# Kernel optimization log

Measured on AMD Instinct MI355X. Metric: run time of the kernel, lower is better.

The kernel has to match this reference:

```python
import jax, jax.numpy as jnp
import numpy as np

NEG_SLOPE = 0.2
EPS = 1e-10

B, N, F_IN = 2, 20000, 128
H, D = 4, 32
E = 640000


def setup_inputs() -> dict:
    key = jax.random.key(0)
    k1, k2, k3, k4, k5 = jax.random.split(key, 5)
    x = jax.random.normal(k1, (B, N, F_IN), dtype=jnp.float32)
    edge_index = jax.random.randint(k2, (2, E), 0, N, dtype=jnp.int64)
    W = jax.random.normal(k3, (H * D, F_IN), dtype=jnp.float32) * (1.0 / np.sqrt(F_IN))
    a_src = jax.random.normal(k4, (H, D), dtype=jnp.float32) * (1.0 / np.sqrt(D))
    a_dst = jax.random.normal(k5, (H, D), dtype=jnp.float32) * (1.0 / np.sqrt(D))
    return {"x": x, "edge_index": edge_index, "W": W, "a_src": a_src, "a_dst": a_dst}


def reference(x, edge_index, W, a_src, a_dst):
    # x: (B, N, F_IN); edge_index: (2, E); W: (H*D, F_IN)
    Bs, Ns, _ = x.shape
    h = (x @ W.T).reshape(Bs, Ns, H, D)          # (B, N, H, D)
    src = edge_index[0]
    dst = edge_index[1]

    h_src = h[:, src]                            # (B, E, H, D) gather
    e_src = jnp.einsum('behd,hd->beh', h_src, a_src)
    e_dst = jnp.einsum('behd,hd->beh', h[:, dst], a_dst)
    e = jax.nn.leaky_relu(e_src + e_dst, NEG_SLOPE)  # (B, E, H)

    # segment softmax over destination nodes (segments on leading axis)
    e_t = jnp.moveaxis(e, 1, 0)                  # (E, B, H)
    max_n = jax.ops.segment_max(e_t, dst, num_segments=Ns)   # (N, B, H)
    exp_e = jnp.exp(e_t - max_n[dst])            # (E, B, H)
    sum_n = jax.ops.segment_sum(exp_e, dst, num_segments=Ns)  # (N, B, H)
    alpha = exp_e / (sum_n[dst] + EPS)           # (E, B, H)

    messages = alpha[..., None] * jnp.moveaxis(h_src, 1, 0)  # (E, B, H, D)
    out = jax.ops.segment_sum(messages, dst, num_segments=Ns)  # (N, B, H, D)
    out = jnp.moveaxis(out, 0, 1).reshape(Bs, Ns, H * D)       # concat heads
    return out
```

## Files before the change

### kernel.cpp

```cpp
#include <hip/hip_runtime.h>
#include <math.h>

#define N_NODES 20000
#define N_B 2
#define N_H 4
#define N_D 32
#define N_F 128
#define N_E 640000
#define BNH (N_B * N_NODES * N_H)

#define GEMM_BLOCKS 625
#define P1_BLOCKS 250
#define EPB 2560
#define NBINS 157
#define NODE_CAP 96
#define TRS 136
#define LOG2E 1.44269504088896f

typedef __attribute__((ext_vector_type(8))) short short8v;
typedef __attribute__((ext_vector_type(4))) float floatx4;

__device__ __forceinline__ unsigned short f2bf(float f) {
  unsigned u = __float_as_uint(f);
  return (unsigned short)((u + 0x7FFFu + ((u >> 16) & 1u)) >> 16);
}

__global__ __launch_bounds__(256) void fused_gemm_p1(
    const float* __restrict__ X, const float* __restrict__ W,
    const int* __restrict__ EI, const float* __restrict__ a_src,
    const float* __restrict__ a_dst, unsigned short* __restrict__ HbI,
    float* __restrict__ sI, float* __restrict__ sdI,
    int* __restrict__ cntB, int* __restrict__ prefB,
    unsigned* __restrict__ blockEdges) {
  __shared__ union {
    struct {
      unsigned short WbS[128 * 128];
      unsigned short Tr[4][16 * TRS];
    } g;
    struct {
      int hist[NBINS];
      int pref[NBINS];
      int wsum[4];
      unsigned buf[EPB];
    } p;
  } sm;
  const int tid = threadIdx.x;

  if (blockIdx.x >= GEMM_BLOCKS) {
    const int pb = blockIdx.x - GEMM_BLOCKS;
    const int e0 = pb * EPB;
    for (int t = tid; t < NBINS; t += 256) sm.p.hist[t] = 0;
    __syncthreads();
    for (int k = 0; k < EPB; k += 256) {
      const int d = EI[N_E + e0 + k + tid];
      atomicAdd(&sm.p.hist[d >> 7], 1);
    }
    __syncthreads();
    {
      const int w = tid >> 6, lane = tid & 63;
      int v = 0, incl = 0;
      if (tid < NBINS) v = sm.p.hist[tid];
      if (w < 3) {
        incl = v;
#pragma unroll
        for (int off = 1; off < 64; off <<= 1) {
          int t2 = __shfl_up(incl, off);
          if (lane >= off) incl += t2;
        }
        if (lane == 63) sm.p.wsum[w] = incl;
      }
      __syncthreads();
      if (tid < NBINS) {
        int add = 0;
        if (w >= 1) add += sm.p.wsum[0];
        if (w >= 2) add += sm.p.wsum[1];
        sm.p.pref[tid] = incl - v + add;
      }
      __syncthreads();
    }
    for (int t = tid; t < NBINS; t += 256) {
      cntB[pb * NBINS + t] = sm.p.hist[t];
      prefB[pb * NBINS + t] = sm.p.pref[t];
      sm.p.hist[t] = sm.p.pref[t];
    }
    __syncthreads();
    for (int k = 0; k < EPB; k += 256) {
      const int i = e0 + k + tid;
      const int d = EI[N_E + i];
      const int s = EI[i];
      const int pos = atomicAdd(&sm.p.hist[d >> 7], 1);
      sm.p.buf[pos] = (unsigned)(((d & 127) << 16) | s);
    }
    __syncthreads();
    for (int k = tid; k < EPB; k += 256)
      blockEdges[(size_t)pb * EPB + k] = sm.p.buf[k];
    return;
  }

  {
    const int o = tid >> 1;
    const int khalf = (tid & 1) * 64;
#pragma unroll
    for (int c = 0; c < 8; ++c) {
      const int k0 = khalf + c * 8;
      const float4 w0 = *(const float4*)&W[(size_t)o * 128 + k0];
      const float4 w1 = *(const float4*)&W[(size_t)o * 128 + k0 + 4];
      union { unsigned short us[8]; uint4 v; } pk;
      pk.us[0] = f2bf(w0.x); pk.us[1] = f2bf(w0.y);
      pk.us[2] = f2bf(w0.z); pk.us[3] = f2bf(w0.w);
      pk.us[4] = f2bf(w1.x); pk.us[5] = f2bf(w1.y);
      pk.us[6] = f2bf(w1.z); pk.us[7] = f2bf(w1.w);
      const int chunk = (k0 >> 3) ^ (o & 15);
      *(uint4*)&sm.g.WbS[o * 128 + chunk * 8] = pk.v;
    }
  }
  __syncthreads();

  const int wv = tid >> 6, lane = tid & 63;
  const int l15 = lane & 15;
  const int row0 = blockIdx.x * 64 + wv * 16;
  const int arow = row0 + l15;
  const int kg = lane >> 4;

  float as[8], ad[8];
#pragma unroll
  for (int cf = 0; cf < 8; ++cf) {
    as[cf] = a_src[cf * 16 + l15];
    ad[cf] = a_dst[cf * 16 + l15];
  }

  short8v afr[4];
#pragma unroll
  for (int kc = 0; kc < 4; ++kc) {
    const size_t xb = (size_t)arow * 128 + kc * 32 + kg * 8;
    const float4 x0 = *(const float4*)&X[xb];
    const float4 x1 = *(const float4*)&X[xb + 4];
    afr[kc][0] = (short)f2bf(x0.x); afr[kc][1] = (short)f2bf(x0.y);
    afr[kc][2] = (short)f2bf(x0.z); afr[kc][3] = (short)f2bf(x0.w);
    afr[kc][4] = (short)f2bf(x1.x); afr[kc][5] = (short)f2bf(x1.y);
    afr[kc][6] = (short)f2bf(x1.z); afr[kc][7] = (short)f2bf(x1.w);
  }

  floatx4 acc[8];
#pragma unroll
  for (int cf = 0; cf < 8; ++cf) acc[cf] = (floatx4){0.f, 0.f, 0.f, 0.f};

#pragma unroll
  for (int kc = 0; kc < 4; ++kc) {
#pragma unroll
    for (int cf = 0; cf < 8; ++cf) {
      const int o = cf * 16 + l15;
      const int chunk = (kc * 4 + kg) ^ l15;
      const short8v bfr = *(const short8v*)&sm.g.WbS[o * 128 + chunk * 8];
      acc[cf] = __builtin_amdgcn_mfma_f32_16x16x32_bf16(afr[kc], bfr, acc[cf], 0, 0, 0);
    }
  }

  {
    float ps[4][4], pd[4][4];
#pragma unroll
    for (int j = 0; j < 4; ++j)
#pragma unroll
      for (int h = 0; h < 4; ++h) {
        float vs = acc[2 * h][j] * as[2 * h] + acc[2 * h + 1][j] * as[2 * h + 1];
        float vd = acc[2 * h][j] * ad[2 * h] + acc[2 * h + 1][j] * ad[2 * h + 1];
#pragma unroll
        for (int m = 1; m <= 8; m <<= 1) {
          vs += __shfl_xor(vs, m);
          vd += __shfl_xor(vd, m);
        }
        ps[j][h] = vs * LOG2E; pd[j][h] = vd * LOG2E;
      }
    if (l15 == 0) {
#pragma unroll
      for (int j = 0; j < 4; ++j) {
        const int m = row0 + kg * 4 + j;
        const int node = (m < N_NODES) ? m : m - N_NODES;
        const int boff = (m < N_NODES) ? 0 : 4;
#pragma unroll
        for (int h = 0; h < 4; ++h) {
          sI[node * 8 + boff + h] = ps[j][h];
          sdI[node * 8 + boff + h] = pd[j][h];
        }
      }
    }
  }

#pragma unroll
  for (int cf = 0; cf < 8; ++cf)
#pragma unroll
    for (int j = 0; j < 4; ++j)
      sm.g.Tr[wv][((kg << 2) + j) * TRS + cf * 16 + l15] = f2bf(acc[cf][j]);
#pragma unroll
  for (int it = 0; it < 4; ++it) {
    const int r = it * 4 + kg;
    const int m = row0 + r;
    const size_t base2 =
        (m < N_NODES) ? (size_t)m * 256 : (size_t)(m - N_NODES) * 256 + 128;
    const uint4 v = *(const uint4*)&sm.g.Tr[wv][r * TRS + l15 * 8];
    *(uint4*)&HbI[base2 + l15 * 8] = v;
  }
}

__global__ __launch_bounds__(256) void bin_kernel(
    const unsigned* __restrict__ blockEdges, const int* __restrict__ cntB,
    const int* __restrict__ prefB, unsigned short* __restrict__ bucket,
    int* __restrict__ count) {
  __shared__ unsigned short list[128][NODE_CAP];
  __shared__ int cnt[128];
  const int bin = blockIdx.x;
  const int tid = threadIdx.x;
  if (tid < 128) cnt[tid] = 0;
  __syncthreads();
  for (int b = tid; b < P1_BLOCKS; b += 256) {
    const int c = cntB[b * NBINS + bin];
    const int p0 = prefB[b * NBINS + bin];
    const size_t base = (size_t)b * EPB + p0;
    for (int q = 0; q < c; ++q) {
      const unsigned u = blockEdges[base + q];
      const int dl = (int)(u >> 16);
      const int r = atomicAdd(&cnt[dl], 1);
      if (r < NODE_CAP) list[dl][r] = (unsigned short)(u & 0xFFFFu);
    }
  }
  __syncthreads();
  const int dl = tid >> 1, half = tid & 1;
  const int node = bin * 128 + dl;
  if (node < N_NODES) {
    const int c = min(cnt[dl], NODE_CAP);
    if (half == 0) count[node] = c;
#pragma unroll
    for (int q = 0; q < 6; ++q) {
      const int off = (half * 6 + q) * 8;
      if (off < c)
        *(uint4*)&bucket[(size_t)node * NODE_CAP + off] =
            *(const uint4*)&list[dl][off];
    }
  }
}

__global__ __launch_bounds__(256) void agg_kernel(
    const uint4* __restrict__ Hu4, const float* __restrict__ sI,
    const float* __restrict__ sdI, const int* __restrict__ count,
    const unsigned short* __restrict__ bucket, float* __restrict__ out) {
  const int node = blockIdx.x * 4 + (threadIdx.x >> 6);
  const int lane = threadIdx.x & 63;
  const int half = lane >> 5;
  const int q = lane & 31;
  const int j = ((q >> 4) << 2) | ((q & 15) >> 2);

  const int cnt = count[node];
  const float sd = sdI[node * 8 + j];
  const int bbase = node * NODE_CAP;

  float den = 0.f;
  float acc[8];
#pragma unroll
  for (int k = 0; k < 8; ++k) acc[k] = 0.f;

#define PCOMP(f_, h_, v_)                                            \
  {                                                                  \
    float lg = (f_) + sd;                                            \
    lg = fmaxf(lg, 0.2f * lg);                                       \
    const float p = (v_) ? exp2f(lg) : 0.f;                          \
    den += p;                                                        \
    acc[0] = fmaf(p, __uint_as_float((h_).x << 16), acc[0]);         \
    acc[1] = fmaf(p, __uint_as_float((h_).x & 0xFFFF0000u), acc[1]); \
    acc[2] = fmaf(p, __uint_as_float((h_).y << 16), acc[2]);         \
    acc[3] = fmaf(p, __uint_as_float((h_).y & 0xFFFF0000u), acc[3]); \
    acc[4] = fmaf(p, __uint_as_float((h_).z << 16), acc[4]);         \
    acc[5] = fmaf(p, __uint_as_float((h_).z & 0xFFFF0000u), acc[5]); \
    acc[6] = fmaf(p, __uint_as_float((h_).w << 16), acc[6]);         \
    acc[7] = fmaf(p, __uint_as_float((h_).w & 0xFFFF0000u), acc[7]); \
  }

  for (int cb = 0; cb < cnt; cb += 64) {
    const int c = min(cnt - cb, 64);
    const int vE = (lane < c) ? (int)bucket[bbase + cb + lane] : 0;
    int e = 0;
    for (; e + 8 <= c; e += 8) {
      const int s0 = __shfl(vE, e + half);
      const int s1 = __shfl(vE, e + 2 + half);
      const int s2 = __shfl(vE, e + 4 + half);
      const int s3 = __shfl(vE, e + 6 + half);
      const uint4 h0 = Hu4[((unsigned)s0 << 5) + q];
      const uint4 h1 = Hu4[((unsigned)s1 << 5) + q];
      const uint4 h2 = Hu4[((unsigned)s2 << 5) + q];
      const uint4 h3 = Hu4[((unsigned)s3 << 5) + q];
      const float f0 = sI[s0 * 8 + j];
      const float f1 = sI[s1 * 8 + j];
      const float f2 = sI[s2 * 8 + j];
      const float f3 = sI[s3 * 8 + j];
      PCOMP(f0, h0, true) PCOMP(f1, h1, true)
      PCOMP(f2, h2, true) PCOMP(f3, h3, true)
    }
    for (; e < c; e += 2) {
      const int idx = e + half;
      const bool v = idx < c;
      const int s0 = __shfl(vE, v ? idx : 0);
      const uint4 h0 = Hu4[((unsigned)s0 << 5) + q];
      const float f0 = sI[s0 * 8 + j];
      PCOMP(f0, h0, v)
    }
  }
#undef PCOMP

  den += __shfl_xor(den, 32);
#pragma unroll
  for (int k = 0; k < 8; ++k) acc[k] += __shfl_xor(acc[k], 32);

  if (lane < 32) {
    const float inv = 1.f / (den + 1e-10f);
    const int b = q >> 4, f0 = (q & 15) * 8;
    float4 o0, o1;
    o0.x = acc[0] * inv; o0.y = acc[1] * inv;
    o0.z = acc[2] * inv; o0.w = acc[3] * inv;
    o1.x = acc[4] * inv; o1.y = acc[5] * inv;
    o1.z = acc[6] * inv; o1.w = acc[7] * inv;
    float* op = &out[(size_t)b * (N_NODES * 128) + (size_t)node * 128 + f0];
    *(float4*)op = o0;
    *(float4*)(op + 4) = o1;
  }
}

extern "C" void kernel_launch(void* const* d_in, const int* in_sizes, int n_in,
                              void* d_out, int out_size, void* d_ws, size_t ws_size,
                              hipStream_t stream) {
  const float* X = (const float*)d_in[0];
  const int* EI = (const int*)d_in[1];
  const float* W = (const float*)d_in[2];
  const float* a_src = (const float*)d_in[3];
  const float* a_dst = (const float*)d_in[4];
  float* out = (float*)d_out;

  unsigned short* hbI = (unsigned short*)d_ws;
  float* sI = (float*)(hbI + (size_t)N_B * N_NODES * N_F);
  float* sdI = sI + BNH;
  int* cntB = (int*)(sdI + BNH);
  int* prefB = cntB + P1_BLOCKS * NBINS;
  unsigned* blockEdges = (unsigned*)(prefB + P1_BLOCKS * NBINS);
  int* count = (int*)(blockEdges + (size_t)N_E);
  unsigned short* bucket = (unsigned short*)(count + N_NODES);

  fused_gemm_p1<<<GEMM_BLOCKS + P1_BLOCKS, 256, 0, stream>>>(
      X, W, EI, a_src, a_dst, hbI, sI, sdI, cntB, prefB, blockEdges);
  bin_kernel<<<NBINS, 256, 0, stream>>>(blockEdges, cntB, prefB, bucket, count);
  agg_kernel<<<N_NODES / 4, 256, 0, stream>>>(
      (const uint4*)hbI, sI, sdI, count, bucket, out);
}
```

Measured before the change: 77.31 us.

## Split hidden features per batch and aggregate each batch in separate blocks

The bf16 projected features are now stored batch-major ([B][N][128]) instead of interleaved per node. The aggregation kernel launches twice as many blocks, each handling one batch, with every lane loading 8 bytes instead of 16 and keeping 4 accumulators instead of 8. The goal is to raise parallelism and occupancy and cut register pressure in the gather-bound aggregation. The cost is that edge indices and bucket reads are done twice, once per batch, and each gathered row segment is smaller.

```diff
diff --git a/kernel.cpp b/kernel.cpp
--- a/kernel.cpp
+++ b/kernel.cpp
@@ -28,7 +28,7 @@
 __global__ __launch_bounds__(256) void fused_gemm_p1(
     const float* __restrict__ X, const float* __restrict__ W,
     const int* __restrict__ EI, const float* __restrict__ a_src,
-    const float* __restrict__ a_dst, unsigned short* __restrict__ HbI,
+    const float* __restrict__ a_dst, unsigned short* __restrict__ Hb,
     float* __restrict__ sI, float* __restrict__ sdI,
     int* __restrict__ cntB, int* __restrict__ prefB,
     unsigned* __restrict__ blockEdges) {
@@ -195,10 +195,8 @@
   for (int it = 0; it < 4; ++it) {
     const int r = it * 4 + kg;
     const int m = row0 + r;
-    const size_t base2 =
-        (m < N_NODES) ? (size_t)m * 256 : (size_t)(m - N_NODES) * 256 + 128;
     const uint4 v = *(const uint4*)&sm.g.Tr[wv][r * TRS + l15 * 8];
-    *(uint4*)&HbI[base2 + l15 * 8] = v;
+    *(uint4*)&Hb[(size_t)m * 128 + l15 * 8] = v;
   }
 }
 
@@ -240,23 +238,25 @@
 }
 
 __global__ __launch_bounds__(256) void agg_kernel(
-    const uint4* __restrict__ Hu4, const float* __restrict__ sI,
+    const unsigned short* __restrict__ Hb, const float* __restrict__ sI,
     const float* __restrict__ sdI, const int* __restrict__ count,
     const unsigned short* __restrict__ bucket, float* __restrict__ out) {
-  const int node = blockIdx.x * 4 + (threadIdx.x >> 6);
+  const int b = blockIdx.x & 1;
+  const int node = (blockIdx.x >> 1) * 4 + (threadIdx.x >> 6);
   const int lane = threadIdx.x & 63;
   const int half = lane >> 5;
   const int q = lane & 31;
-  const int j = ((q >> 4) << 2) | ((q & 15) >> 2);
+  const int j = b * 4 + (q >> 3);
+
+  const uint2* __restrict__ Hb2 =
+      (const uint2*)Hb + (size_t)b * N_NODES * 32;
 
   const int cnt = count[node];
   const float sd = sdI[node * 8 + j];
   const int bbase = node * NODE_CAP;
 
   float den = 0.f;
-  float acc[8];
-#pragma unroll
-  for (int k = 0; k < 8; ++k) acc[k] = 0.f;
+  float a0 = 0.f, a1 = 0.f, a2 = 0.f, a3 = 0.f;
 
 #define PCOMP(f_, h_, v_)                                            \
   {                                                                  \
@@ -264,14 +264,10 @@
     lg = fmaxf(lg, 0.2f * lg);                                       \
     const float p = (v_) ? exp2f(lg) : 0.f;                          \
     den += p;                                                        \
-    acc[0] = fmaf(p, __uint_as_float((h_).x << 16), acc[0]);         \
-    acc[1] = fmaf(p, __uint_as_float((h_).x & 0xFFFF0000u), acc[1]); \
-    acc[2] = fmaf(p, __uint_as_float((h_).y << 16), acc[2]);         \
-    acc[3] = fmaf(p, __uint_as_float((h_).y & 0xFFFF0000u), acc[3]); \
-    acc[4] = fmaf(p, __uint_as_float((h_).z << 16), acc[4]);         \
-    acc[5] = fmaf(p, __uint_as_float((h_).z & 0xFFFF0000u), acc[5]); \
-    acc[6] = fmaf(p, __uint_as_float((h_).w << 16), acc[6]);         \
-    acc[7] = fmaf(p, __uint_as_float((h_).w & 0xFFFF0000u), acc[7]); \
+    a0 = fmaf(p, __uint_as_float((h_).x << 16), a0);                 \
+    a1 = fmaf(p, __uint_as_float((h_).x & 0xFFFF0000u), a1);         \
+    a2 = fmaf(p, __uint_as_float((h_).y << 16), a2);                 \
+    a3 = fmaf(p, __uint_as_float((h_).y & 0xFFFF0000u), a3);         \
   }
 
   for (int cb = 0; cb < cnt; cb += 64) {
@@ -283,10 +279,10 @@
       const int s1 = __shfl(vE, e + 2 + half);
       const int s2 = __shfl(vE, e + 4 + half);
       const int s3 = __shfl(vE, e + 6 + half);
-      const uint4 h0 = Hu4[((unsigned)s0 << 5) + q];
-      const uint4 h1 = Hu4[((unsigned)s1 << 5) + q];
-      const uint4 h2 = Hu4[((unsigned)s2 << 5) + q];
-      const uint4 h3 = Hu4[((unsigned)s3 << 5) + q];
+      const uint2 h0 = Hb2[((unsigned)s0 << 5) + q];
+      const uint2 h1 = Hb2[((unsigned)s1 << 5) + q];
+      const uint2 h2 = Hb2[((unsigned)s2 << 5) + q];
+      const uint2 h3 = Hb2[((unsigned)s3 << 5) + q];
       const float f0 = sI[s0 * 8 + j];
       const float f1 = sI[s1 * 8 + j];
       const float f2 = sI[s2 * 8 + j];
@@ -298,7 +294,7 @@
       const int idx = e + half;
       const bool v = idx < c;
       const int s0 = __shfl(vE, v ? idx : 0);
-      const uint4 h0 = Hu4[((unsigned)s0 << 5) + q];
+      const uint2 h0 = Hb2[((unsigned)s0 << 5) + q];
       const float f0 = sI[s0 * 8 + j];
       PCOMP(f0, h0, v)
     }
@@ -306,20 +302,16 @@
 #undef PCOMP
 
   den += __shfl_xor(den, 32);
-#pragma unroll
-  for (int k = 0; k < 8; ++k) acc[k] += __shfl_xor(acc[k], 32);
+  a0 += __shfl_xor(a0, 32);
+  a1 += __shfl_xor(a1, 32);
+  a2 += __shfl_xor(a2, 32);
+  a3 += __shfl_xor(a3, 32);
 
   if (lane < 32) {
     const float inv = 1.f / (den + 1e-10f);
-    const int b = q >> 4, f0 = (q & 15) * 8;
-    float4 o0, o1;
-    o0.x = acc[0] * inv; o0.y = acc[1] * inv;
-    o0.z = acc[2] * inv; o0.w = acc[3] * inv;
-    o1.x = acc[4] * inv; o1.y = acc[5] * inv;
-    o1.z = acc[6] * inv; o1.w = acc[7] * inv;
-    float* op = &out[(size_t)b * (N_NODES * 128) + (size_t)node * 128 + f0];
-    *(float4*)op = o0;
-    *(float4*)(op + 4) = o1;
+    float4 o;
+    o.x = a0 * inv; o.y = a1 * inv; o.z = a2 * inv; o.w = a3 * inv;
+    *(float4*)&out[(size_t)b * (N_NODES * 128) + (size_t)node * 128 + q * 4] = o;
   }
 }
 
@@ -333,8 +325,8 @@
   const float* a_dst = (const float*)d_in[4];
   float* out = (float*)d_out;
 
-  unsigned short* hbI = (unsigned short*)d_ws;
-  float* sI = (float*)(hbI + (size_t)N_B * N_NODES * N_F);
+  unsigned short* hb = (unsigned short*)d_ws;
+  float* sI = (float*)(hb + (size_t)N_B * N_NODES * N_F);
   float* sdI = sI + BNH;
   int* cntB = (int*)(sdI + BNH);
   int* prefB = cntB + P1_BLOCKS * NBINS;
@@ -343,8 +335,8 @@
   unsigned short* bucket = (unsigned short*)(count + N_NODES);
 
   fused_gemm_p1<<<GEMM_BLOCKS + P1_BLOCKS, 256, 0, stream>>>(
-      X, W, EI, a_src, a_dst, hbI, sI, sdI, cntB, prefB, blockEdges);
+      X, W, EI, a_src, a_dst, hb, sI, sdI, cntB, prefB, blockEdges);
   bin_kernel<<<NBINS, 256, 0, stream>>>(blockEdges, cntB, prefB, bucket, count);
-  agg_kernel<<<N_NODES / 4, 256, 0, stream>>>(
-      (const uint4*)hbI, sI, sdI, count, bucket, out);
-}
+  agg_kernel<<<(N_NODES / 4) * 2, 256, 0, stream>>>(hb, sI, sdI, count, bucket,
+                                                    out);
+}
```

Measured after the change: 73.17 us. 5.4% less time.
